# Performance work log

Measured on AMD Instinct MI355X. Metric: run time of the kernel, lower is better.

## Reference

```python
import jax, jax.numpy as jnp
import numpy as np

VOCAB = 100000
EMBED = 128
BATCH = 1024
SEQ = 200
EPS = 1e-12  # F.normalize eps


def setup_inputs() -> dict:
    key = jax.random.key(0)
    k_x, k_emb, k_wi, k_bi, k_wh, k_bh = jax.random.split(key, 6)
    x = jax.random.randint(k_x, (BATCH, SEQ), 0, VOCAB, dtype=jnp.int32)
    emb_table = jax.random.normal(k_emb, (VOCAB, EMBED), dtype=jnp.float32) * 0.02
    emb_table = emb_table.at[0].set(0.0)  # padding_idx=0
    lim = 1.0 / np.sqrt(EMBED)
    W_in = jax.random.uniform(k_wi, (EMBED, EMBED), jnp.float32, -lim, lim)
    b_in = jax.random.uniform(k_bi, (EMBED,), jnp.float32, -lim, lim)
    W_h = jax.random.uniform(k_wh, (EMBED, EMBED), jnp.float32, -lim, lim)
    b_h = jax.random.uniform(k_bh, (EMBED,), jnp.float32, -lim, lim)
    return {"x": x, "emb_table": emb_table, "W_in": W_in, "b_in": b_in,
            "W_h": W_h, "b_h": b_h}


def reference(x, emb_table, W_in, b_in, W_h, b_h):
    emb = emb_table[x]  # [B, S, E]
    # precompute input projection for all timesteps: [B, S, E]
    inp_proj = jnp.einsum('bse,fe->bsf', emb, W_in) + b_in
    h0 = jnp.zeros((emb.shape[0], emb.shape[2]), emb.dtype)

    def step(h, ip_t):  # ip_t: [B, E]
        h_new = jnp.tanh(ip_t + h @ W_h.T + b_h)
        return h_new, None

    h, _ = jax.lax.scan(step, h0, jnp.swapaxes(inp_proj, 0, 1))  # scan over S
    # dropout is identity in eval mode; L2-normalize along dim 1
    norm = jnp.linalg.norm(h, axis=1, keepdims=True)
    return h / jnp.maximum(norm, EPS)
```

## Files before the change

### kernel.cpp

```cpp
#include <hip/hip_runtime.h>

#define BATCH 1024
#define SEQ   200
#define EMB   128
#define VOCAB 100000

typedef __attribute__((ext_vector_type(8))) short short8;
typedef __attribute__((ext_vector_type(4))) float f32x4;
typedef _Float16 hh2 __attribute__((ext_vector_type(2)));

__device__ __forceinline__ unsigned short f2bf(float x) {
  unsigned u = __float_as_uint(x);
  u += 0x7fffu + ((u >> 16) & 1u);
  return (unsigned short)(u >> 16);
}
__device__ __forceinline__ float bf2f(unsigned short b) {
  return __uint_as_float(((unsigned)b) << 16);
}
__device__ __forceinline__ unsigned int packh2(float a, float b) {
  const hh2 p = (hh2){(_Float16)a, (_Float16)b};
  return __builtin_bit_cast(unsigned int, p);
}
__device__ __forceinline__ float fd(unsigned int h2, unsigned int w2, float acc) {
  return __builtin_amdgcn_fdot2(__builtin_bit_cast(hh2, h2),
                                __builtin_bit_cast(hh2, w2), acc, false);
}

__global__ __launch_bounds__(256) void cvt_all(
    const float* __restrict__ Win, const float* __restrict__ Wh,
    unsigned short* __restrict__ Wb, uint4* __restrict__ W4) {
  const int idx = blockIdx.x * 256 + threadIdx.x;
  if (idx < 16384) {
    Wb[idx] = f2bf(Win[idx]);
  } else {
    const int j = idx - 16384;
    const int c = j >> 7;
    const int f = j & 127;
    const float* wr = Wh + (size_t)f * EMB;
    uint4 o;
    o.x = packh2(wr[4*c + 0], wr[4*c + 64]);
    o.y = packh2(wr[4*c + 1], wr[4*c + 65]);
    o.z = packh2(wr[4*c + 2], wr[4*c + 66]);
    o.w = packh2(wr[4*c + 3], wr[4*c + 67]);
    W4[j] = o;
  }
}

__global__ __launch_bounds__(256) void proj2(
    const int* __restrict__ xidx, const float* __restrict__ emb,
    const unsigned short* __restrict__ Wb, unsigned int* __restrict__ ipP)
{
  const int tid = threadIdx.x;
  const int w   = tid >> 6;
  const int l   = tid & 63;
  const int l15 = l & 15;
  const int lhi = l >> 4;

  short8 bfrag[8][4];
#pragma unroll
  for (int nt = 0; nt < 8; ++nt)
#pragma unroll
    for (int kc = 0; kc < 4; ++kc)
      bfrag[nt][kc] = *(const short8*)(Wb + (nt*16 + l15)*EMB + kc*32 + lhi*8);

#pragma unroll
  for (int t = 0; t < 2; ++t) {
    const int m  = blockIdx.x*8 + w*2 + t;
    const int rb = m * 16;
    const long xe = (long)xidx[rb + l15] * EMB;
    short8 afrag[4];
#pragma unroll
    for (int kc = 0; kc < 4; ++kc) {
      const float4* p = (const float4*)(emb + xe + kc*32 + lhi*8);
      float4 a = p[0], b = p[1];
      short8 fr;
      fr[0]=(short)f2bf(a.x); fr[1]=(short)f2bf(a.y);
      fr[2]=(short)f2bf(a.z); fr[3]=(short)f2bf(a.w);
      fr[4]=(short)f2bf(b.x); fr[5]=(short)f2bf(b.y);
      fr[6]=(short)f2bf(b.z); fr[7]=(short)f2bf(b.w);
      afrag[kc] = fr;
    }
    f32x4 acc[8];
#pragma unroll
    for (int nt = 0; nt < 8; ++nt) acc[nt] = (f32x4)(0.0f);
#pragma unroll
    for (int kc = 0; kc < 4; ++kc)
#pragma unroll
      for (int nt = 0; nt < 8; ++nt)
        acc[nt] = __builtin_amdgcn_mfma_f32_16x16x32_bf16(afrag[kc], bfrag[nt][kc], acc[nt], 0, 0, 0);
#pragma unroll
    for (int nt = 0; nt < 4; ++nt)
#pragma unroll
      for (int j = 0; j < 4; ++j) {
        const unsigned int u = (unsigned)f2bf(acc[nt][j])
                             | ((unsigned)f2bf(acc[nt+4][j]) << 16);
        ipP[(long)(rb + lhi*4 + j)*64 + nt*16 + l15] = u;
      }
  }
}

__global__ __attribute__((amdgpu_waves_per_eu(1, 1)))
__launch_bounds__(256) void rnn17(
    const unsigned int* __restrict__ ipP, const uint4* __restrict__ W4,
    const float* __restrict__ bin, const float* __restrict__ bh,
    float* __restrict__ out)
{
  __shared__ unsigned int hb[4][2][64];

  const int tid = threadIdx.x;
  const int w   = tid >> 6;
  const int l   = tid & 63;
  const int row = blockIdx.x*4 + w;

  hb[w][0][l] = 0u;

#define WLD(i) \
  const uint4 wa##i = W4[(i)*128 + l]; \
  const uint4 wb##i = W4[(i)*128 + 64 + l];
  WLD(0)  WLD(1)  WLD(2)  WLD(3)  WLD(4)  WLD(5)  WLD(6)  WLD(7)
  WLD(8)  WLD(9)  WLD(10) WLD(11) WLD(12) WLD(13) WLD(14) WLD(15)
#undef WLD

  const float bias0 = bin[l]      + bh[l];
  const float bias1 = bin[l + 64] + bh[l + 64];
  __syncthreads();

  const unsigned int* ipp = ipP + (size_t)row * SEQ * 64 + l;
  unsigned int ic = ipp[0];
  unsigned int in = ipp[64];

  float hf0 = 0.0f, hf1 = 0.0f;

  for (int s = 0; s < SEQ; ++s) {
    const int sp = (s + 2 < SEQ) ? s + 2 : SEQ - 1;
    const unsigned int pn = ipp[(size_t)sp * 64];

    const uint4* th = (const uint4*)&hb[w][s & 1][0];

    float a00 = bias0 + __uint_as_float(ic << 16);
    float a10 = bias1 + __uint_as_float(ic & 0xffff0000u);
    float a01 = 0.0f, a02 = 0.0f, a03 = 0.0f;
    float a11 = 0.0f, a12 = 0.0f, a13 = 0.0f;

#define STEP(i, K) { \
    const uint4 hc = th[i]; \
    a0##K = fd(hc.x, wa##i.x, a0##K); \
    a0##K = fd(hc.y, wa##i.y, a0##K); \
    a0##K = fd(hc.z, wa##i.z, a0##K); \
    a0##K = fd(hc.w, wa##i.w, a0##K); \
    a1##K = fd(hc.x, wb##i.x, a1##K); \
    a1##K = fd(hc.y, wb##i.y, a1##K); \
    a1##K = fd(hc.z, wb##i.z, a1##K); \
    a1##K = fd(hc.w, wb##i.w, a1##K); }
    STEP(0,0)  STEP(1,1)  STEP(2,2)  STEP(3,3)
    STEP(4,0)  STEP(5,1)  STEP(6,2)  STEP(7,3)
    STEP(8,0)  STEP(9,1)  STEP(10,2) STEP(11,3)
    STEP(12,0) STEP(13,1) STEP(14,2) STEP(15,3)
#undef STEP

    const float v0 = (a00 + a01) + (a02 + a03);
    const float v1 = (a10 + a11) + (a12 + a13);

    const float e0 = __expf(2.0f * v0);
    hf0 = 1.0f - __fdividef(2.0f, e0 + 1.0f);
    const float e1 = __expf(2.0f * v1);
    hf1 = 1.0f - __fdividef(2.0f, e1 + 1.0f);

    hb[w][(s + 1) & 1][l] = packh2(hf0, hf1);

    ic = in;
    in = pn;
  }

  float pj = hf0*hf0 + hf1*hf1;
#pragma unroll
  for (int off = 1; off < 64; off <<= 1) pj += __shfl_xor(pj, off, 64);
  const float inv = 1.0f / fmaxf(sqrtf(pj), 1e-12f);
  out[(size_t)row*EMB + l]      = hf0 * inv;
  out[(size_t)row*EMB + 64 + l] = hf1 * inv;
}

__global__ __launch_bounds__(512) void rnn_fused(
    const int* __restrict__ xidx, const float* __restrict__ emb,
    const float* __restrict__ Win, const float* __restrict__ bin,
    const float* __restrict__ Wh,  const float* __restrict__ bh,
    float* __restrict__ out)
{
  __shared__ float h_lds[4][EMB];
  __shared__ float part[8][4][EMB];
  __shared__ float emb_lds[2][4][EMB];
  __shared__ int   x_lds[4][SEQ];
  __shared__ float red[8];

  const int t   = threadIdx.x;
  const int f0  = (t & 63) * 2;
  const int eg  = t >> 6;
  const int e0  = eg * 16;
  const int b0  = blockIdx.x * 4;
  const int row = t >> 7;
  const int ff  = t & 127;

  float wh0[16], wh1[16], wi0[16], wi1[16];
  {
    const float* p0 = Wh + f0*EMB + e0;
    const float* p1 = Wh + (f0+1)*EMB + e0;
    const float* q0 = Win + f0*EMB + e0;
    const float* q1 = Win + (f0+1)*EMB + e0;
#pragma unroll
    for (int q = 0; q < 4; ++q) {
      float4 a = ((const float4*)p0)[q];
      wh0[4*q+0]=a.x; wh0[4*q+1]=a.y; wh0[4*q+2]=a.z; wh0[4*q+3]=a.w;
      float4 b = ((const float4*)p1)[q];
      wh1[4*q+0]=b.x; wh1[4*q+1]=b.y; wh1[4*q+2]=b.z; wh1[4*q+3]=b.w;
      float4 c = ((const float4*)q0)[q];
      wi0[4*q+0]=c.x; wi0[4*q+1]=c.y; wi0[4*q+2]=c.z; wi0[4*q+3]=c.w;
      float4 d = ((const float4*)q1)[q];
      wi1[4*q+0]=d.x; wi1[4*q+1]=d.y; wi1[4*q+2]=d.z; wi1[4*q+3]=d.w;
    }
  }
  const float bc = bin[ff] + bh[ff];
  h_lds[row][ff] = 0.0f;
  for (int i = t; i < 4*SEQ; i += 512)
    x_lds[i / SEQ][i % SEQ] = xidx[(b0 + i/SEQ)*SEQ + (i % SEQ)];
  __syncthreads();
  emb_lds[0][row][ff] = emb[(long)x_lds[row][0]*EMB + ff];
  __syncthreads();

  int cur = 0;
  for (int s = 0; s < SEQ; ++s) {
    float nxt = 0.0f;
    if (s + 1 < SEQ) nxt = emb[(long)x_lds[row][s+1]*EMB + ff];
    float pa0[4], pa1[4];
#pragma unroll
    for (int rq = 0; rq < 4; ++rq) { pa0[rq] = 0.0f; pa1[rq] = 0.0f; }
#pragma unroll
    for (int rq = 0; rq < 4; ++rq) {
      const float4* hp  = (const float4*)&h_lds[rq][e0];
      const float4* epv = (const float4*)&emb_lds[cur][rq][e0];
#pragma unroll
      for (int q = 0; q < 4; ++q) {
        float4 hv = hp[q], ev = epv[q];
        pa0[rq] = fmaf(hv.x, wh0[4*q+0], pa0[rq]); pa0[rq] = fmaf(hv.y, wh0[4*q+1], pa0[rq]);
        pa0[rq] = fmaf(hv.z, wh0[4*q+2], pa0[rq]); pa0[rq] = fmaf(hv.w, wh0[4*q+3], pa0[rq]);
        pa1[rq] = fmaf(hv.x, wh1[4*q+0], pa1[rq]); pa1[rq] = fmaf(hv.y, wh1[4*q+1], pa1[rq]);
        pa1[rq] = fmaf(hv.z, wh1[4*q+2], pa1[rq]); pa1[rq] = fmaf(hv.w, wh1[4*q+3], pa1[rq]);
        pa0[rq] = fmaf(ev.x, wi0[4*q+0], pa0[rq]); pa0[rq] = fmaf(ev.y, wi0[4*q+1], pa0[rq]);
        pa0[rq] = fmaf(ev.z, wi0[4*q+2], pa0[rq]); pa0[rq] = fmaf(ev.w, wi0[4*q+3], pa0[rq]);
        pa1[rq] = fmaf(ev.x, wi1[4*q+0], pa1[rq]); pa1[rq] = fmaf(ev.y, wi1[4*q+1], pa1[rq]);
        pa1[rq] = fmaf(ev.z, wi1[4*q+2], pa1[rq]); pa1[rq] = fmaf(ev.w, wi1[4*q+3], pa1[rq]);
      }
    }
#pragma unroll
    for (int rq = 0; rq < 4; ++rq) {
      part[eg][rq][f0]   = pa0[rq];
      part[eg][rq][f0+1] = pa1[rq];
    }
    __syncthreads();
    float acc = bc;
#pragma unroll
    for (int g = 0; g < 8; ++g) acc += part[g][row][ff];
    float hn = tanhf(acc);
    if (s + 1 < SEQ) emb_lds[cur ^ 1][row][ff] = nxt;
    h_lds[row][ff] = hn;
    __syncthreads();
    cur ^= 1;
  }
  float hv = h_lds[row][ff];
  float sq = hv * hv;
#pragma unroll
  for (int off = 32; off > 0; off >>= 1) sq += __shfl_xor(sq, off, 64);
  if ((t & 63) == 0) red[t >> 6] = sq;
  __syncthreads();
  float nrm = sqrtf(red[row*2] + red[row*2 + 1]);
  out[(b0 + row)*EMB + ff] = hv / fmaxf(nrm, 1e-12f);
}

extern "C" void kernel_launch(void* const* d_in, const int* in_sizes, int n_in,
                              void* d_out, int out_size, void* d_ws, size_t ws_size,
                              hipStream_t stream) {
  const int*   x    = (const int*)  d_in[0];
  const float* emb  = (const float*)d_in[1];
  const float* Win  = (const float*)d_in[2];
  const float* bin  = (const float*)d_in[3];
  const float* Wh   = (const float*)d_in[4];
  const float* bh   = (const float*)d_in[5];
  float* out = (float*)d_out;

  const size_t ip_bytes = (size_t)BATCH * SEQ * 64 * sizeof(unsigned int);
  const size_t wb_bytes = (size_t)EMB * EMB * sizeof(unsigned short);
  const size_t w4_bytes = (size_t)16 * 128 * sizeof(uint4);
  const size_t need     = ip_bytes + wb_bytes + w4_bytes;
  if (ws_size >= need) {
    unsigned int*   ipP = (unsigned int*)d_ws;
    unsigned short* Wb  = (unsigned short*)((char*)d_ws + ip_bytes);
    uint4*          W4  = (uint4*)((char*)d_ws + ip_bytes + wb_bytes);
    cvt_all<<<72, 256, 0, stream>>>(Win, Wh, Wb, W4);
    proj2<<<(BATCH*SEQ)/128, 256, 0, stream>>>(x, emb, Wb, ipP);
    rnn17<<<BATCH/4, 256, 0, stream>>>(ipP, W4, bin, bh, out);
  } else {
    rnn_fused<<<BATCH/4, 512, 0, stream>>>(x, emb, Win, bin, Wh, bh, out);
  }
}
```

Measured before the change: 142.9 us.

## Split projection output columns across waves to cut per-thread W registers

```diff
diff --git a/kernel.cpp b/kernel.cpp
--- a/kernel.cpp
+++ b/kernel.cpp
@@ -46,7 +46,7 @@
   }
 }
 
-__global__ __launch_bounds__(256) void proj2(
+__global__ __launch_bounds__(256) void proj3(
     const int* __restrict__ xidx, const float* __restrict__ emb,
     const unsigned short* __restrict__ Wb, unsigned int* __restrict__ ipP)
 {
@@ -56,17 +56,18 @@
   const int l15 = l & 15;
   const int lhi = l >> 4;
 
-  short8 bfrag[8][4];
-#pragma unroll
-  for (int nt = 0; nt < 8; ++nt)
-#pragma unroll
-    for (int kc = 0; kc < 4; ++kc)
-      bfrag[nt][kc] = *(const short8*)(Wb + (nt*16 + l15)*EMB + kc*32 + lhi*8);
-
-#pragma unroll
-  for (int t = 0; t < 2; ++t) {
-    const int m  = blockIdx.x*8 + w*2 + t;
-    const int rb = m * 16;
+  short8 b0[4], b1[4];
+#pragma unroll
+  for (int kc = 0; kc < 4; ++kc) {
+    b0[kc] = *(const short8*)(Wb + (w*16       + l15)*EMB + kc*32 + lhi*8);
+    b1[kc] = *(const short8*)(Wb + ((w+4)*16   + l15)*EMB + kc*32 + lhi*8);
+  }
+
+  const int rb0 = blockIdx.x * 32;
+
+#pragma unroll
+  for (int mt = 0; mt < 2; ++mt) {
+    const int rb = rb0 + mt*16;
     const long xe = (long)xidx[rb + l15] * EMB;
     short8 afrag[4];
 #pragma unroll
@@ -80,22 +81,18 @@
       fr[6]=(short)f2bf(b.z); fr[7]=(short)f2bf(b.w);
       afrag[kc] = fr;
     }
-    f32x4 acc[8];
-#pragma unroll
-    for (int nt = 0; nt < 8; ++nt) acc[nt] = (f32x4)(0.0f);
-#pragma unroll
-    for (int kc = 0; kc < 4; ++kc)
-#pragma unroll
-      for (int nt = 0; nt < 8; ++nt)
-        acc[nt] = __builtin_amdgcn_mfma_f32_16x16x32_bf16(afrag[kc], bfrag[nt][kc], acc[nt], 0, 0, 0);
-#pragma unroll
-    for (int nt = 0; nt < 4; ++nt)
-#pragma unroll
-      for (int j = 0; j < 4; ++j) {
-        const unsigned int u = (unsigned)f2bf(acc[nt][j])
-                             | ((unsigned)f2bf(acc[nt+4][j]) << 16);
-        ipP[(long)(rb + lhi*4 + j)*64 + nt*16 + l15] = u;
-      }
+    f32x4 a0 = (f32x4)(0.0f), a1 = (f32x4)(0.0f);
+#pragma unroll
+    for (int kc = 0; kc < 4; ++kc) {
+      a0 = __builtin_amdgcn_mfma_f32_16x16x32_bf16(afrag[kc], b0[kc], a0, 0, 0, 0);
+      a1 = __builtin_amdgcn_mfma_f32_16x16x32_bf16(afrag[kc], b1[kc], a1, 0, 0, 0);
+    }
+#pragma unroll
+    for (int j = 0; j < 4; ++j) {
+      const unsigned int u = (unsigned)f2bf(a0[j])
+                           | ((unsigned)f2bf(a1[j]) << 16);
+      ipP[(long)(rb + lhi*4 + j)*64 + w*16 + l15] = u;
+    }
   }
 }
 
@@ -295,7 +292,7 @@
     unsigned short* Wb  = (unsigned short*)((char*)d_ws + ip_bytes);
     uint4*          W4  = (uint4*)((char*)d_ws + ip_bytes + wb_bytes);
     cvt_all<<<72, 256, 0, stream>>>(Win, Wh, Wb, W4);
-    proj2<<<(BATCH*SEQ)/128, 256, 0, stream>>>(x, emb, Wb, ipP);
+    proj3<<<(BATCH*SEQ)/32, 256, 0, stream>>>(x, emb, Wb, ipP);
     rnn17<<<BATCH/4, 256, 0, stream>>>(ipP, W4, bin, bh, out);
   } else {
     rnn_fused<<<BATCH/4, 512, 0, stream>>>(x, emb, Win, bin, Wh, bh, out);
```

Result: slower. 170.3 us (+19.1%).
